# Kernel optimization log

Measured on AMD Instinct MI355X. Metric: run time of the kernel, lower is better.

## Reference

```python
import jax, jax.numpy as jnp
import numpy as np

B, S, D_MODEL, H = 4, 2048, 2048, 16
HD = D_MODEL // H  # 128
ROPE_BASE = 10000.0


def apply_rope(x):
    # x: [B, H, S, HD]; interleaved-pair rotary embedding along seq axis
    s, d = x.shape[2], x.shape[3]
    inv_freq = 1.0 / (ROPE_BASE ** (jnp.arange(0, d, 2, dtype=jnp.float32) / d))  # [d/2]
    ang = jnp.arange(s, dtype=jnp.float32)[:, None] * inv_freq[None, :]  # [S, d/2]
    cos, sin = jnp.cos(ang), jnp.sin(ang)
    x0, x1 = x[..., 0::2], x[..., 1::2]  # [B,H,S,d/2]
    o0 = x0 * cos - x1 * sin
    o1 = x0 * sin + x1 * cos
    return jnp.stack([o0, o1], axis=-1).reshape(x.shape)


def setup_inputs() -> dict:
    key = jax.random.key(0)
    ks = jax.random.split(key, 5)
    sc = 1.0 / np.sqrt(D_MODEL)
    return {
        "x": jax.random.normal(ks[0], (B, S, D_MODEL), dtype=jnp.float32),
        "Wq": jax.random.normal(ks[1], (D_MODEL, D_MODEL), dtype=jnp.float32) * sc,
        "Wk": jax.random.normal(ks[2], (D_MODEL, D_MODEL), dtype=jnp.float32) * sc,
        "Wv": jax.random.normal(ks[3], (D_MODEL, D_MODEL), dtype=jnp.float32) * sc,
        "Wo": jax.random.normal(ks[4], (D_MODEL, D_MODEL), dtype=jnp.float32) * sc,
        "bo": jnp.zeros((D_MODEL,), dtype=jnp.float32),
    }


def reference(x, Wq, Wk, Wv, Wo, bo):
    b, s, _ = x.shape
    # torch Linear: y = x @ W.T (no qkv bias)
    q = (x @ Wq.T).reshape(b, s, H, HD).transpose(0, 2, 1, 3)  # [B,H,S,HD]
    k = (x @ Wk.T).reshape(b, s, H, HD).transpose(0, 2, 1, 3)
    v = (x @ Wv.T).reshape(b, s, H, HD).transpose(0, 2, 1, 3)
    q = apply_rope(q)
    k = apply_rope(k)
    scores = jnp.einsum("bhqd,bhkd->bhqk", q, k)
    causal = jnp.tril(jnp.ones((s, s), dtype=bool))
    scores = jnp.where(causal, scores, -jnp.inf)
    attn = jax.nn.softmax(scores / jnp.sqrt(jnp.float32(HD)), axis=-1)
    # dropout p=0.0 -> identity
    ctx = jnp.einsum("bhqk,bhkd->bqhd", attn, v).reshape(b, s, H * HD)
    return ctx @ Wo.T + bo
```

## Files before the change

### kernel.cpp

```cpp
#include <hip/hip_runtime.h>
#include <hip/hip_bf16.h>
#include <math.h>

#define B_  4
#define S_  2048
#define DM  2048
#define H_  16
#define HD_ 128

typedef __bf16 bf16;
typedef __bf16 bf16x4 __attribute__((ext_vector_type(4)));
typedef __bf16 bf16x8 __attribute__((ext_vector_type(8)));
typedef float  f32x4  __attribute__((ext_vector_type(4)));

__device__ __forceinline__ void gload_lds16(const bf16* g, bf16* l) {
  __builtin_amdgcn_global_load_lds(
      (const __attribute__((address_space(1))) void*)g,
      (__attribute__((address_space(3))) void*)l, 16, 0, 0);
}

#define NX4 4194304
#define NW4 1048576
__global__ void cast_all(const float* __restrict__ x, const float* __restrict__ wq,
                         const float* __restrict__ wk, const float* __restrict__ wv,
                         const float* __restrict__ wo,
                         bf16* __restrict__ xb, bf16* __restrict__ wqkv,
                         bf16* __restrict__ wob) {
  const int total = NX4 + 4 * NW4;
  int stride = gridDim.x * blockDim.x;
  for (int i = blockIdx.x * blockDim.x + threadIdx.x; i < total; i += stride) {
    const float* src; bf16* dst; int j;
    if (i < NX4) { src = x; dst = xb; j = i; }
    else {
      int t = i - NX4; int r = t >> 20; j = t & (NW4 - 1);
      if      (r == 0) { src = wq; dst = wqkv; }
      else if (r == 1) { src = wk; dst = wqkv + (size_t)NW4 * 4; }
      else if (r == 2) { src = wv; dst = wqkv + (size_t)NW4 * 8; }
      else             { src = wo; dst = wob; }
    }
    float4 v = reinterpret_cast<const float4*>(src)[j];
    bf16x4 o = { (bf16)v.x, (bf16)v.y, (bf16)v.z, (bf16)v.w };
    reinterpret_cast<bf16x4*>(dst)[j] = o;
  }
}

__global__ void rope_table_k(float* __restrict__ tab) {
  int idx = blockIdx.x * blockDim.x + threadIdx.x;
  if (idx >= S_ * (HD_ / 2)) return;
  int pos = idx >> 6, i = idx & 63;
  float inv = powf(10000.0f, -(2.0f * i) / (float)HD_);
  float ang = (float)pos * inv;
  tab[2 * idx]     = cosf(ang);
  tab[2 * idx + 1] = sinf(ang);
}

template<int EPI>
__global__ __launch_bounds__(512, 2)
void gemm8p(const bf16* __restrict__ A, const bf16* __restrict__ Bt,
            bf16* __restrict__ Oq, bf16* __restrict__ Ok, bf16* __restrict__ Ovt,
            float* __restrict__ Cf, const float* __restrict__ bias,
            const float* __restrict__ tab, int N, int K) {
  __shared__ char lds[131072];
  const int tid = threadIdx.x;
  const int w = tid >> 6, l = tid & 63;
  const int lr = l & 15, lg = l >> 4;
  const int wm = w >> 2, wn = w & 3;
  const int L = blockIdx.x + gridDim.x * blockIdx.y;
  const int xcd = L & 7, s = L >> 3;
  const int rpx = gridDim.y >> 3;
  const int qq_ = s / gridDim.x;
  const int by = xcd * rpx + qq_;
  const int bx = s - qq_ * gridDim.x;
  const int row0 = by * 256, col0 = bx * 256;
  const int NT = K >> 6;

  auto stageSlot = [&](int isB, int kh, int kt2) {
    const bf16* src = isB ? (Bt + (size_t)col0 * K) : (A + (size_t)row0 * K);
    char* dstbase = (char*)lds + (kt2 & 1) * 65536 + isB * 32768 + kh * 16384;
    const int kcol = kt2 * 64 + kh * 32;
#pragma unroll
    for (int u = 0; u < 2; ++u) {
      int D = w * 2048 + u * 1024 + l * 16;
      int r = D >> 6, cb = D & 63;
      int sc = cb ^ (((r >> 1) & 3) << 4);
      gload_lds16(src + (size_t)r * K + kcol + (sc >> 1),
                  (bf16*)(dstbase + w * 2048 + u * 1024));
    }
  };

  const int swzt = ((lr >> 1) & 3) << 4;
  int offA[2][4], offB[4];
#pragma unroll
  for (int qm = 0; qm < 2; ++qm)
#pragma unroll
    for (int mi = 0; mi < 4; ++mi) {
      int r = wm * 128 + qm * 64 + mi * 16 + lr;
      offA[qm][mi] = r * 64 + ((lg * 16) ^ swzt);
    }
#pragma unroll
  for (int ni = 0; ni < 4; ++ni) {
    int r = wn * 64 + ni * 16 + lr;
    offB[ni] = 32768 + r * 64 + ((lg * 16) ^ swzt);
  }

  f32x4 acc[8][4] = {};

  stageSlot(0, 0, 0); stageSlot(1, 0, 0);
  stageSlot(0, 1, 0); stageSlot(1, 1, 0);
  if (NT > 1) { stageSlot(0, 0, 1); stageSlot(1, 0, 1); }

#pragma unroll 1
  for (int kt = 0; kt < NT; ++kt) {
    const char* bufb = (const char*)lds + (kt & 1) * 65536;
#pragma unroll
    for (int q = 0; q < 4; ++q) {
      const int kh = q >> 1;
      const int qmm = (q & 1);
      if (q == 0) {
        if (kt + 1 < NT) asm volatile("s_waitcnt vmcnt(8)" ::: "memory");
        else             asm volatile("s_waitcnt vmcnt(4)" ::: "memory");
        __builtin_amdgcn_s_barrier();
      } else if (q == 2) {
        if (kt + 1 < NT) asm volatile("s_waitcnt vmcnt(8)" ::: "memory");
        else             asm volatile("s_waitcnt vmcnt(0)" ::: "memory");
        __builtin_amdgcn_s_barrier();
      }
      const char* bb = bufb + kh * 16384;
      bf16x8 af[4], bfr[4];
#pragma unroll
      for (int mi = 0; mi < 4; ++mi)
        af[mi] = *reinterpret_cast<const bf16x8*>(bb + offA[qmm][mi]);
#pragma unroll
      for (int ni = 0; ni < 4; ++ni)
        bfr[ni] = *reinterpret_cast<const bf16x8*>(bb + offB[ni]);
      if (q < 2) { if (kt + 1 < NT) stageSlot(q & 1, 1, kt + 1); }
      else       { if (kt + 2 < NT) stageSlot(q & 1, 0, kt + 2); }
      __builtin_amdgcn_s_barrier();
      __builtin_amdgcn_s_setprio(1);
#pragma unroll
      for (int mi = 0; mi < 4; ++mi)
#pragma unroll
        for (int ni = 0; ni < 4; ++ni)
          acc[qmm * 4 + mi][ni] =
              __builtin_amdgcn_mfma_f32_16x16x32_bf16(af[mi], bfr[ni], acc[qmm * 4 + mi][ni], 0, 0, 0);
      __builtin_amdgcn_s_setprio(0);
    }
  }

#pragma unroll
  for (int ai = 0; ai < 8; ++ai) {
    int rb = row0 + wm * 128 + ai * 16 + lg * 4;
#pragma unroll
    for (int ni = 0; ni < 4; ++ni) {
      int gc = col0 + wn * 64 + ni * 16 + lr;
      if (EPI == 1) {
#pragma unroll
        for (int j = 0; j < 4; ++j)
          Cf[(size_t)(rb + j) * N + gc] = acc[ai][ni][j] + bias[gc];
      } else {
        int reg = col0 >> 11;
        int cc = gc & 2047;
        if (reg == 2) {
          int bb2 = rb >> 11, ss = rb & 2047;
          int hh = cc >> 7, dd = cc & 127;
          bf16x4 pack = { (bf16)acc[ai][ni][0], (bf16)acc[ai][ni][1],
                          (bf16)acc[ai][ni][2], (bf16)acc[ai][ni][3] };
          *reinterpret_cast<bf16x4*>(Ovt + (((size_t)(bb2 * H_ + hh) * HD_ + dd) << 11) + ss) = pack;
        } else {
          bf16* Dst = (reg == 0) ? Oq : Ok;
          float scale = (reg == 0) ? 0.08838834764831845f : 1.0f;
          int i2 = (cc & 127) >> 1;
          float sgn = (lr & 1) ? 1.0f : -1.0f;
#pragma unroll
          for (int j = 0; j < 4; ++j) {
            float own = acc[ai][ni][j];
            float par = __shfl_xor(own, 1);
            int ss = (rb + j) & (S_ - 1);
            float2 cs = reinterpret_cast<const float2*>(tab)[ss * 64 + i2];
            Dst[(size_t)(rb + j) * 2048 + cc] = (bf16)((own * cs.x + sgn * par * cs.y) * scale);
          }
        }
      }
    }
  }
}

__global__ __launch_bounds__(512, 4)
void attn_fwd(const bf16* __restrict__ Q, const bf16* __restrict__ K,
              const bf16* __restrict__ Vt, bf16* __restrict__ O) {
  __shared__ bf16 Ks[2][64 * 128];
  __shared__ bf16 Vs[2][128 * 64];
  __shared__ bf16 Ps[8][16 * 64];
  const int tid = threadIdx.x;
  const int w = tid >> 6, l = tid & 63;
  const int lr = l & 15, lg = l >> 4;
  const int L = blockIdx.x + 8 * (blockIdx.y + 16 * blockIdx.z);
  const int xcd = L & 7, s = L >> 3;
  const int p = xcd * 8 + (s & 7);
  const int bx = s >> 3;
  const int h = p & 15, b = p >> 4;
  const size_t bbase = (size_t)b * S_ * DM + (size_t)h * HD_;
  const bf16* vtb = Vt + (size_t)(b * H_ + h) * HD_ * S_;

#pragma unroll 1
  for (int pass = 0; pass < 2; ++pass) {
    const int qt = pass ? bx : (15 - bx);
    const int q0 = qt * 128 + w * 16;
    const int ktmax = 2 * qt + 1;

    bf16x8 qf[4];
#pragma unroll
    for (int kb = 0; kb < 4; ++kb)
      qf[kb] = *reinterpret_cast<const bf16x8*>(Q + bbase + (size_t)(q0 + lr) * DM + kb * 32 + lg * 8);

    float m_r = -INFINITY;
    float l_r = 0.f;
    f32x4 o[8] = {};

#pragma unroll
    for (int i = 0; i < 2; ++i) {
      int X = w * 2048 + i * 1024 + l * 16;
      int r = X >> 8, scb = (X & 255) ^ ((r & 7) << 4);
      gload_lds16(K + bbase + (size_t)r * DM + (scb >> 1), &Ks[0][(w * 2048 + i * 1024) >> 1]);
    }
#pragma unroll
    for (int i = 0; i < 2; ++i) {
      int X = w * 2048 + i * 1024 + l * 16;
      int d = X >> 7, scb = (X & 127) ^ ((d & 7) << 4);
      gload_lds16(vtb + (size_t)d * S_ + (scb >> 1), &Vs[0][(w * 2048 + i * 1024) >> 1]);
    }

    for (int kt = 0; kt <= ktmax; ++kt) {
      const int buf = kt & 1;
      if (kt < ktmax) {
        const int nk = (kt + 1) * 64;
#pragma unroll
        for (int i = 0; i < 2; ++i) {
          int X = w * 2048 + i * 1024 + l * 16;
          int r = X >> 8, scb = (X & 255) ^ ((r & 7) << 4);
          gload_lds16(K + bbase + (size_t)(nk + r) * DM + (scb >> 1),
                      &Ks[buf ^ 1][(w * 2048 + i * 1024) >> 1]);
        }
#pragma unroll
        for (int i = 0; i < 2; ++i) {
          int X = w * 2048 + i * 1024 + l * 16;
          int d = X >> 7, scb = (X & 127) ^ ((d & 7) << 4);
          gload_lds16(vtb + (size_t)d * S_ + nk + (scb >> 1),
                      &Vs[buf ^ 1][(w * 2048 + i * 1024) >> 1]);
        }
        asm volatile("s_waitcnt vmcnt(4)" ::: "memory");
      } else {
        asm volatile("s_waitcnt vmcnt(0)" ::: "memory");
      }
      __builtin_amdgcn_s_barrier();

      f32x4 sc4[4];
      __builtin_amdgcn_s_setprio(1);
#pragma unroll
      for (int cb = 0; cb < 4; ++cb) {
        sc4[cb] = f32x4{0.f, 0.f, 0.f, 0.f};
        int r = cb * 16 + lr;
#pragma unroll
        for (int kb = 0; kb < 4; ++kb) {
          int off = r * 256 + ((kb * 64 + lg * 16) ^ ((lr & 7) << 4));
          bf16x8 kf = *reinterpret_cast<const bf16x8*>((const char*)Ks[buf] + off);
          sc4[cb] = __builtin_amdgcn_mfma_f32_16x16x32_bf16(kf, qf[kb], sc4[cb], 0, 0, 0);
        }
      }
      __builtin_amdgcn_s_setprio(0);

      const int kv0 = kt * 64;
      if (kv0 + 63 > q0) {
        const int qq = q0 + lr;
#pragma unroll
        for (int cb = 0; cb < 4; ++cb)
#pragma unroll
          for (int jj = 0; jj < 4; ++jj)
            if (kv0 + cb * 16 + lg * 4 + jj > qq) sc4[cb][jj] = -INFINITY;
      }

      float tm = -INFINITY;
#pragma unroll
      for (int cb = 0; cb < 4; ++cb)
#pragma unroll
        for (int jj = 0; jj < 4; ++jj) tm = fmaxf(tm, sc4[cb][jj]);
      tm = fmaxf(tm, __shfl_xor(tm, 16));
      tm = fmaxf(tm, __shfl_xor(tm, 32));
      const bool resc = !__all(tm <= m_r + 8.0f);
      float sc_f = 1.f;
      if (resc) {
        float mnew = fmaxf(m_r, tm);
        sc_f = __expf(m_r - mnew);
        m_r = mnew;
      }
      float rs = 0.f;
#pragma unroll
      for (int cb = 0; cb < 4; ++cb)
#pragma unroll
        for (int jj = 0; jj < 4; ++jj) {
          float pp = __expf(sc4[cb][jj] - m_r);
          sc4[cb][jj] = pp;
          rs += pp;
        }
      rs += __shfl_xor(rs, 16);
      rs += __shfl_xor(rs, 32);
      l_r = l_r * sc_f + rs;
      if (resc) {
        float scO[4];
#pragma unroll
        for (int j = 0; j < 4; ++j) scO[j] = __shfl(sc_f, lg * 4 + j);
#pragma unroll
        for (int nb = 0; nb < 8; ++nb)
#pragma unroll
          for (int j = 0; j < 4; ++j) o[nb][j] *= scO[j];
      }

#pragma unroll
      for (int cb = 0; cb < 4; ++cb) {
        bf16x4 pk = { (bf16)sc4[cb][0], (bf16)sc4[cb][1], (bf16)sc4[cb][2], (bf16)sc4[cb][3] };
        int off = lr * 128 + ((cb * 32 + lg * 8) ^ ((lr & 7) << 4));
        *reinterpret_cast<bf16x4*>((char*)Ps[w] + off) = pk;
      }

      bf16x8 pf[2];
#pragma unroll
      for (int kc = 0; kc < 2; ++kc) {
        int off = lr * 128 + ((kc * 64 + lg * 16) ^ ((lr & 7) << 4));
        pf[kc] = *reinterpret_cast<const bf16x8*>((const char*)Ps[w] + off);
      }
      __builtin_amdgcn_s_setprio(1);
#pragma unroll
      for (int nb = 0; nb < 8; ++nb) {
        int d = nb * 16 + lr;
#pragma unroll
        for (int kc = 0; kc < 2; ++kc) {
          int off = d * 128 + ((kc * 64 + lg * 16) ^ ((lr & 7) << 4));
          bf16x8 vf = *reinterpret_cast<const bf16x8*>((const char*)Vs[buf] + off);
          o[nb] = __builtin_amdgcn_mfma_f32_16x16x32_bf16(pf[kc], vf, o[nb], 0, 0, 0);
        }
      }
      __builtin_amdgcn_s_setprio(0);

      asm volatile("s_waitcnt lgkmcnt(0)" ::: "memory");
      __builtin_amdgcn_s_barrier();
    }

    float lO[4];
#pragma unroll
    for (int j = 0; j < 4; ++j) lO[j] = __shfl(l_r, lg * 4 + j);
#pragma unroll
    for (int j = 0; j < 4; ++j) {
      float inv = 1.0f / lO[j];
      size_t rowoff = bbase + (size_t)(q0 + lg * 4 + j) * DM;
#pragma unroll
      for (int nb = 0; nb < 8; ++nb)
        O[rowoff + nb * 16 + lr] = (bf16)(o[nb][j] * inv);
    }
  }
}

extern "C" void kernel_launch(void* const* d_in, const int* in_sizes, int n_in,
                              void* d_out, int out_size, void* d_ws, size_t ws_size,
                              hipStream_t stream) {
  const float* x  = (const float*)d_in[0];
  const float* Wq = (const float*)d_in[1];
  const float* Wk = (const float*)d_in[2];
  const float* Wv = (const float*)d_in[3];
  const float* Wo = (const float*)d_in[4];
  const float* bo = (const float*)d_in[5];
  float* out = (float*)d_out;

  const size_t NX = (size_t)B_ * S_ * DM;
  const size_t NW = (size_t)DM * DM;
  char* ws = (char*)d_ws;
  bf16* xb   = (bf16*)ws; ws += NX * 2;
  bf16* wqkv = (bf16*)ws; ws += 3 * NW * 2;
  bf16* wob  = (bf16*)ws; ws += NW * 2;
  bf16* qb   = (bf16*)ws; ws += NX * 2;
  bf16* kb   = (bf16*)ws; ws += NX * 2;
  bf16* vt   = (bf16*)ws; ws += NX * 2;
  bf16* ctxb = (bf16*)ws; ws += NX * 2;
  float* tab = (float*)ws; ws += (size_t)S_ * 64 * 2 * sizeof(float);

  cast_all<<<2048, 256, 0, stream>>>(x, Wq, Wk, Wv, Wo, xb, wqkv, wob);
  rope_table_k<<<(S_ * 64 + 255) / 256, 256, 0, stream>>>(tab);

  const int M = B_ * S_;
  gemm8p<0><<<dim3(3 * DM / 256, M / 256), 512, 0, stream>>>(
      xb, wqkv, qb, kb, vt, nullptr, nullptr, tab, 3 * DM, DM);

  attn_fwd<<<dim3(8, H_, B_), 512, 0, stream>>>(qb, kb, vt, ctxb);

  gemm8p<1><<<dim3(DM / 256, M / 256), 512, 0, stream>>>(
      ctxb, wob, nullptr, nullptr, nullptr, out, bo, nullptr, DM, DM);
}
```

Baseline: 418.4 us.

## Switch GEMMs to 32x32x16 MFMA with full-K-tile staging and simpler pipeline

Both projection GEMMs now use 32x32x16 bf16 MFMA tiles instead of 16x16x32, which cuts the number of LDS fragment reads per MFMA. Each K-tile of 64 is staged as a whole, with a 128-byte row swizzle and a simpler two-phase double buffer. The XCD-aware block remapping is dropped in favour of plain blockIdx ordering. The trade-off is less prefetch depth (one tile ahead instead of two half-tiles) and possibly worse L2 locality, since blocks are no longer grouped per XCD.

```diff
diff --git a/kernel.cpp b/kernel.cpp
--- a/kernel.cpp
+++ b/kernel.cpp
@@ -12,6 +12,7 @@
 typedef __bf16 bf16x4 __attribute__((ext_vector_type(4)));
 typedef __bf16 bf16x8 __attribute__((ext_vector_type(8)));
 typedef float  f32x4  __attribute__((ext_vector_type(4)));
+typedef float  f32x16 __attribute__((ext_vector_type(16)));
 
 __device__ __forceinline__ void gload_lds16(const bf16* g, bf16* l) {
   __builtin_amdgcn_global_load_lds(
@@ -56,133 +57,133 @@
 
 template<int EPI>
 __global__ __launch_bounds__(512, 2)
-void gemm8p(const bf16* __restrict__ A, const bf16* __restrict__ Bt,
+void gemm32(const bf16* __restrict__ A, const bf16* __restrict__ Bt,
             bf16* __restrict__ Oq, bf16* __restrict__ Ok, bf16* __restrict__ Ovt,
             float* __restrict__ Cf, const float* __restrict__ bias,
             const float* __restrict__ tab, int N, int K) {
   __shared__ char lds[131072];
   const int tid = threadIdx.x;
   const int w = tid >> 6, l = tid & 63;
-  const int lr = l & 15, lg = l >> 4;
+  const int l31 = l & 31, lh = l >> 5;
   const int wm = w >> 2, wn = w & 3;
-  const int L = blockIdx.x + gridDim.x * blockIdx.y;
-  const int xcd = L & 7, s = L >> 3;
-  const int rpx = gridDim.y >> 3;
-  const int qq_ = s / gridDim.x;
-  const int by = xcd * rpx + qq_;
-  const int bx = s - qq_ * gridDim.x;
-  const int row0 = by * 256, col0 = bx * 256;
+  const int row0 = blockIdx.y * 256, col0 = blockIdx.x * 256;
   const int NT = K >> 6;
 
-  auto stageSlot = [&](int isB, int kh, int kt2) {
+  auto stageOp = [&](int isB, int kt2) {
     const bf16* src = isB ? (Bt + (size_t)col0 * K) : (A + (size_t)row0 * K);
-    char* dstbase = (char*)lds + (kt2 & 1) * 65536 + isB * 32768 + kh * 16384;
-    const int kcol = kt2 * 64 + kh * 32;
-#pragma unroll
-    for (int u = 0; u < 2; ++u) {
-      int D = w * 2048 + u * 1024 + l * 16;
-      int r = D >> 6, cb = D & 63;
-      int sc = cb ^ (((r >> 1) & 3) << 4);
-      gload_lds16(src + (size_t)r * K + kcol + (sc >> 1),
-                  (bf16*)(dstbase + w * 2048 + u * 1024));
+    char* dst = (char*)lds + (kt2 & 1) * 65536 + isB * 32768 + w * 4096;
+    const int kc = kt2 * 64;
+#pragma unroll
+    for (int g = 0; g < 4; ++g) {
+      int D = w * 4096 + g * 1024 + l * 16;
+      int r = D >> 7, cb = D & 127;
+      int sc = cb ^ ((r & 7) << 4);
+      gload_lds16(src + (size_t)r * K + kc + (sc >> 1), (bf16*)(dst + g * 1024));
     }
   };
 
-  const int swzt = ((lr >> 1) & 3) << 4;
-  int offA[2][4], offB[4];
-#pragma unroll
-  for (int qm = 0; qm < 2; ++qm)
-#pragma unroll
-    for (int mi = 0; mi < 4; ++mi) {
-      int r = wm * 128 + qm * 64 + mi * 16 + lr;
-      offA[qm][mi] = r * 64 + ((lg * 16) ^ swzt);
-    }
-#pragma unroll
-  for (int ni = 0; ni < 4; ++ni) {
-    int r = wn * 64 + ni * 16 + lr;
-    offB[ni] = 32768 + r * 64 + ((lg * 16) ^ swzt);
-  }
-
-  f32x4 acc[8][4] = {};
-
-  stageSlot(0, 0, 0); stageSlot(1, 0, 0);
-  stageSlot(0, 1, 0); stageSlot(1, 1, 0);
-  if (NT > 1) { stageSlot(0, 0, 1); stageSlot(1, 0, 1); }
+  int rA[4], sA[4], rB[2], sB[2];
+#pragma unroll
+  for (int mi = 0; mi < 4; ++mi) {
+    int r = wm * 128 + mi * 32 + l31;
+    rA[mi] = r * 128; sA[mi] = (r & 7) << 4;
+  }
+#pragma unroll
+  for (int ni = 0; ni < 2; ++ni) {
+    int r = wn * 64 + ni * 32 + l31;
+    rB[ni] = 32768 + r * 128; sB[ni] = (r & 7) << 4;
+  }
+  const int kbase = lh * 16;
+
+  f32x16 acc[4][2] = {};
+
+  stageOp(0, 0); stageOp(1, 0);
 
 #pragma unroll 1
   for (int kt = 0; kt < NT; ++kt) {
     const char* bufb = (const char*)lds + (kt & 1) * 65536;
 #pragma unroll
-    for (int q = 0; q < 4; ++q) {
-      const int kh = q >> 1;
-      const int qmm = (q & 1);
-      if (q == 0) {
-        if (kt + 1 < NT) asm volatile("s_waitcnt vmcnt(8)" ::: "memory");
-        else             asm volatile("s_waitcnt vmcnt(4)" ::: "memory");
+    for (int p = 0; p < 2; ++p) {
+      if (p == 0) {
+        if (kt + 1 < NT) { stageOp(0, kt + 1); asm volatile("s_waitcnt vmcnt(4)" ::: "memory"); }
+        else             { asm volatile("s_waitcnt vmcnt(0)" ::: "memory"); }
         __builtin_amdgcn_s_barrier();
-      } else if (q == 2) {
-        if (kt + 1 < NT) asm volatile("s_waitcnt vmcnt(8)" ::: "memory");
-        else             asm volatile("s_waitcnt vmcnt(0)" ::: "memory");
-        __builtin_amdgcn_s_barrier();
-      }
-      const char* bb = bufb + kh * 16384;
-      bf16x8 af[4], bfr[4];
+      } else {
+        if (kt + 1 < NT) stageOp(1, kt + 1);
+      }
+      bf16x8 af[4][2], bfv[2][2];
 #pragma unroll
       for (int mi = 0; mi < 4; ++mi)
-        af[mi] = *reinterpret_cast<const bf16x8*>(bb + offA[qmm][mi]);
-#pragma unroll
-      for (int ni = 0; ni < 4; ++ni)
-        bfr[ni] = *reinterpret_cast<const bf16x8*>(bb + offB[ni]);
-      if (q < 2) { if (kt + 1 < NT) stageSlot(q & 1, 1, kt + 1); }
-      else       { if (kt + 2 < NT) stageSlot(q & 1, 0, kt + 2); }
-      __builtin_amdgcn_s_barrier();
+#pragma unroll
+        for (int ks = 0; ks < 2; ++ks)
+          af[mi][ks] = *reinterpret_cast<const bf16x8*>(
+              bufb + rA[mi] + ((p * 64 + ks * 32 + kbase) ^ sA[mi]));
+#pragma unroll
+      for (int ni = 0; ni < 2; ++ni)
+#pragma unroll
+        for (int ks = 0; ks < 2; ++ks)
+          bfv[ni][ks] = *reinterpret_cast<const bf16x8*>(
+              bufb + rB[ni] + ((p * 64 + ks * 32 + kbase) ^ sB[ni]));
       __builtin_amdgcn_s_setprio(1);
 #pragma unroll
       for (int mi = 0; mi < 4; ++mi)
 #pragma unroll
-        for (int ni = 0; ni < 4; ++ni)
-          acc[qmm * 4 + mi][ni] =
-              __builtin_amdgcn_mfma_f32_16x16x32_bf16(af[mi], bfr[ni], acc[qmm * 4 + mi][ni], 0, 0, 0);
+        for (int ni = 0; ni < 2; ++ni)
+#pragma unroll
+          for (int ks = 0; ks < 2; ++ks)
+            acc[mi][ni] = __builtin_amdgcn_mfma_f32_32x32x16_bf16(
+                af[mi][ks], bfv[ni][ks], acc[mi][ni], 0, 0, 0);
       __builtin_amdgcn_s_setprio(0);
-    }
-  }
-
-#pragma unroll
-  for (int ai = 0; ai < 8; ++ai) {
-    int rb = row0 + wm * 128 + ai * 16 + lg * 4;
-#pragma unroll
-    for (int ni = 0; ni < 4; ++ni) {
-      int gc = col0 + wn * 64 + ni * 16 + lr;
+      if (p == 1) __builtin_amdgcn_s_barrier();
+    }
+  }
+
+#pragma unroll
+  for (int mi = 0; mi < 4; ++mi)
+#pragma unroll
+    for (int ni = 0; ni < 2; ++ni) {
+      int gc = col0 + wn * 64 + ni * 32 + l31;
       if (EPI == 1) {
 #pragma unroll
-        for (int j = 0; j < 4; ++j)
-          Cf[(size_t)(rb + j) * N + gc] = acc[ai][ni][j] + bias[gc];
+        for (int g = 0; g < 4; ++g) {
+          int rbase = row0 + wm * 128 + mi * 32 + 8 * g + 4 * lh;
+#pragma unroll
+          for (int j = 0; j < 4; ++j)
+            Cf[(size_t)(rbase + j) * N + gc] = acc[mi][ni][4 * g + j] + bias[gc];
+        }
       } else {
         int reg = col0 >> 11;
         int cc = gc & 2047;
         if (reg == 2) {
-          int bb2 = rb >> 11, ss = rb & 2047;
           int hh = cc >> 7, dd = cc & 127;
-          bf16x4 pack = { (bf16)acc[ai][ni][0], (bf16)acc[ai][ni][1],
-                          (bf16)acc[ai][ni][2], (bf16)acc[ai][ni][3] };
-          *reinterpret_cast<bf16x4*>(Ovt + (((size_t)(bb2 * H_ + hh) * HD_ + dd) << 11) + ss) = pack;
+#pragma unroll
+          for (int g = 0; g < 4; ++g) {
+            int rbase = row0 + wm * 128 + mi * 32 + 8 * g + 4 * lh;
+            int bb2 = rbase >> 11, ss = rbase & 2047;
+            bf16x4 pack = { (bf16)acc[mi][ni][4 * g], (bf16)acc[mi][ni][4 * g + 1],
+                            (bf16)acc[mi][ni][4 * g + 2], (bf16)acc[mi][ni][4 * g + 3] };
+            *reinterpret_cast<bf16x4*>(Ovt + (((size_t)(bb2 * H_ + hh) * HD_ + dd) << 11) + ss) = pack;
+          }
         } else {
           bf16* Dst = (reg == 0) ? Oq : Ok;
           float scale = (reg == 0) ? 0.08838834764831845f : 1.0f;
           int i2 = (cc & 127) >> 1;
-          float sgn = (lr & 1) ? 1.0f : -1.0f;
-#pragma unroll
-          for (int j = 0; j < 4; ++j) {
-            float own = acc[ai][ni][j];
-            float par = __shfl_xor(own, 1);
-            int ss = (rb + j) & (S_ - 1);
-            float2 cs = reinterpret_cast<const float2*>(tab)[ss * 64 + i2];
-            Dst[(size_t)(rb + j) * 2048 + cc] = (bf16)((own * cs.x + sgn * par * cs.y) * scale);
+          float sgn = (l & 1) ? 1.0f : -1.0f;
+#pragma unroll
+          for (int g = 0; g < 4; ++g) {
+            int rbase = row0 + wm * 128 + mi * 32 + 8 * g + 4 * lh;
+#pragma unroll
+            for (int j = 0; j < 4; ++j) {
+              float own = acc[mi][ni][4 * g + j];
+              float par = __shfl_xor(own, 1);
+              int ss = (rbase + j) & (S_ - 1);
+              float2 cs = reinterpret_cast<const float2*>(tab)[ss * 64 + i2];
+              Dst[(size_t)(rbase + j) * 2048 + cc] = (bf16)((own * cs.x + sgn * par * cs.y) * scale);
+            }
           }
         }
       }
     }
-  }
 }
 
 __global__ __launch_bounds__(512, 4)
@@ -386,11 +387,11 @@
   rope_table_k<<<(S_ * 64 + 255) / 256, 256, 0, stream>>>(tab);
 
   const int M = B_ * S_;
-  gemm8p<0><<<dim3(3 * DM / 256, M / 256), 512, 0, stream>>>(
+  gemm32<0><<<dim3(3 * DM / 256, M / 256), 512, 0, stream>>>(
       xb, wqkv, qb, kb, vt, nullptr, nullptr, tab, 3 * DM, DM);
 
   attn_fwd<<<dim3(8, H_, B_), 512, 0, stream>>>(qb, kb, vt, ctxb);
 
-  gemm8p<1><<<dim3(DM / 256, M / 256), 512, 0, stream>>>(
+  gemm32<1><<<dim3(DM / 256, M / 256), 512, 0, stream>>>(
       ctxb, wob, nullptr, nullptr, nullptr, out, bo, nullptr, DM, DM);
 }
```

New measurement: 422.2 us. About the same (+0.9%).

## Restructure GEMM k-loop to reuse B fragments and drop XCD block remap

Applied to the files above, without the earlier changes.

The GEMM main loop now walks two k-halves per tile instead of four quarters. Each half loads the B fragments from LDS once and reuses them for both M sub-tiles, with the A-fragment reload and the next global-to-LDS stage interleaved between the two MFMA groups. The vmcnt waits and barriers move to match the new stage order. The XCD-aware block-index remapping is replaced by plain blockIdx tiling, which may reduce L2 locality across chiplets.

```diff
diff --git a/kernel.cpp b/kernel.cpp
--- a/kernel.cpp
+++ b/kernel.cpp
@@ -56,22 +56,16 @@
 
 template<int EPI>
 __global__ __launch_bounds__(512, 2)
-void gemm8p(const bf16* __restrict__ A, const bf16* __restrict__ Bt,
-            bf16* __restrict__ Oq, bf16* __restrict__ Ok, bf16* __restrict__ Ovt,
-            float* __restrict__ Cf, const float* __restrict__ bias,
-            const float* __restrict__ tab, int N, int K) {
+void gemm16d(const bf16* __restrict__ A, const bf16* __restrict__ Bt,
+             bf16* __restrict__ Oq, bf16* __restrict__ Ok, bf16* __restrict__ Ovt,
+             float* __restrict__ Cf, const float* __restrict__ bias,
+             const float* __restrict__ tab, int N, int K) {
   __shared__ char lds[131072];
   const int tid = threadIdx.x;
   const int w = tid >> 6, l = tid & 63;
   const int lr = l & 15, lg = l >> 4;
   const int wm = w >> 2, wn = w & 3;
-  const int L = blockIdx.x + gridDim.x * blockIdx.y;
-  const int xcd = L & 7, s = L >> 3;
-  const int rpx = gridDim.y >> 3;
-  const int qq_ = s / gridDim.x;
-  const int by = xcd * rpx + qq_;
-  const int bx = s - qq_ * gridDim.x;
-  const int row0 = by * 256, col0 = bx * 256;
+  const int row0 = blockIdx.y * 256, col0 = blockIdx.x * 256;
   const int NT = K >> 6;
 
   auto stageSlot = [&](int isB, int kh, int kt2) {
@@ -108,41 +102,53 @@
   stageSlot(0, 0, 0); stageSlot(1, 0, 0);
   stageSlot(0, 1, 0); stageSlot(1, 1, 0);
   if (NT > 1) { stageSlot(0, 0, 1); stageSlot(1, 0, 1); }
+  asm volatile("s_waitcnt vmcnt(8)" ::: "memory");
+  __builtin_amdgcn_s_barrier();
 
 #pragma unroll 1
   for (int kt = 0; kt < NT; ++kt) {
     const char* bufb = (const char*)lds + (kt & 1) * 65536;
 #pragma unroll
-    for (int q = 0; q < 4; ++q) {
-      const int kh = q >> 1;
-      const int qmm = (q & 1);
-      if (q == 0) {
-        if (kt + 1 < NT) asm volatile("s_waitcnt vmcnt(8)" ::: "memory");
-        else             asm volatile("s_waitcnt vmcnt(4)" ::: "memory");
-        __builtin_amdgcn_s_barrier();
-      } else if (q == 2) {
-        if (kt + 1 < NT) asm volatile("s_waitcnt vmcnt(8)" ::: "memory");
-        else             asm volatile("s_waitcnt vmcnt(0)" ::: "memory");
-        __builtin_amdgcn_s_barrier();
-      }
+    for (int kh = 0; kh < 2; ++kh) {
       const char* bb = bufb + kh * 16384;
       bf16x8 af[4], bfr[4];
 #pragma unroll
-      for (int mi = 0; mi < 4; ++mi)
-        af[mi] = *reinterpret_cast<const bf16x8*>(bb + offA[qmm][mi]);
-#pragma unroll
       for (int ni = 0; ni < 4; ++ni)
         bfr[ni] = *reinterpret_cast<const bf16x8*>(bb + offB[ni]);
-      if (q < 2) { if (kt + 1 < NT) stageSlot(q & 1, 1, kt + 1); }
-      else       { if (kt + 2 < NT) stageSlot(q & 1, 0, kt + 2); }
+#pragma unroll
+      for (int mi = 0; mi < 4; ++mi)
+        af[mi] = *reinterpret_cast<const bf16x8*>(bb + offA[0][mi]);
+      if (kh == 0) { if (kt + 1 < NT) stageSlot(0, 1, kt + 1); }
+      else         { if (kt + 2 < NT) stageSlot(0, 0, kt + 2); }
       __builtin_amdgcn_s_barrier();
       __builtin_amdgcn_s_setprio(1);
 #pragma unroll
       for (int mi = 0; mi < 4; ++mi)
 #pragma unroll
         for (int ni = 0; ni < 4; ++ni)
-          acc[qmm * 4 + mi][ni] =
-              __builtin_amdgcn_mfma_f32_16x16x32_bf16(af[mi], bfr[ni], acc[qmm * 4 + mi][ni], 0, 0, 0);
+          acc[mi][ni] = __builtin_amdgcn_mfma_f32_16x16x32_bf16(af[mi], bfr[ni], acc[mi][ni], 0, 0, 0);
+      __builtin_amdgcn_s_setprio(0);
+#pragma unroll
+      for (int mi = 0; mi < 4; ++mi)
+        af[mi] = *reinterpret_cast<const bf16x8*>(bb + offA[1][mi]);
+      if (kh == 0) {
+        if (kt + 1 < NT) stageSlot(1, 1, kt + 1);
+        if (kt == NT - 1) asm volatile("s_waitcnt vmcnt(0)" ::: "memory");
+        else              asm volatile("s_waitcnt vmcnt(8)" ::: "memory");
+      } else {
+        if (kt + 2 < NT) stageSlot(1, 0, kt + 2);
+        if (kt < NT - 1) {
+          if (kt == NT - 2) asm volatile("s_waitcnt vmcnt(4)" ::: "memory");
+          else              asm volatile("s_waitcnt vmcnt(8)" ::: "memory");
+        }
+      }
+      __builtin_amdgcn_s_barrier();
+      __builtin_amdgcn_s_setprio(1);
+#pragma unroll
+      for (int mi = 0; mi < 4; ++mi)
+#pragma unroll
+        for (int ni = 0; ni < 4; ++ni)
+          acc[4 + mi][ni] = __builtin_amdgcn_mfma_f32_16x16x32_bf16(af[mi], bfr[ni], acc[4 + mi][ni], 0, 0, 0);
       __builtin_amdgcn_s_setprio(0);
     }
   }
@@ -386,11 +392,11 @@
   rope_table_k<<<(S_ * 64 + 255) / 256, 256, 0, stream>>>(tab);
 
   const int M = B_ * S_;
-  gemm8p<0><<<dim3(3 * DM / 256, M / 256), 512, 0, stream>>>(
+  gemm16d<0><<<dim3(3 * DM / 256, M / 256), 512, 0, stream>>>(
       xb, wqkv, qb, kb, vt, nullptr, nullptr, tab, 3 * DM, DM);
 
   attn_fwd<<<dim3(8, H_, B_), 512, 0, stream>>>(qb, kb, vt, ctxb);
 
-  gemm8p<1><<<dim3(DM / 256, M / 256), 512, 0, stream>>>(
+  gemm16d<1><<<dim3(DM / 256, M / 256), 512, 0, stream>>>(
       ctxb, wob, nullptr, nullptr, nullptr, out, bo, nullptr, DM, DM);
 }
```

Measured after the change: 402.7 us (median of 3 runs). -3.8%, faster.

## Restructure GEMM main loop into two-tile phases with register-held B fragments

Applied to the files above, without the earlier changes.

Rewrites the GEMM pipeline so each loop iteration processes two K-tiles in eight phases. B fragments stay in registers across four phases, and the LDS layout is changed to 128-byte rows with an XOR swizzle. The load schedule is staggered across phases, and the XCD-aware block remapping is removed in favour of plain blockIdx mapping. This aims to cut redundant LDS reads of B and smooth how global loads overlap with MFMA work. In exchange it adds an extra barrier and an lgkmcnt wait per phase, and may lose L2 locality from the dropped block swizzle.

```diff
diff --git a/kernel.cpp b/kernel.cpp
--- a/kernel.cpp
+++ b/kernel.cpp
@@ -56,7 +56,7 @@
 
 template<int EPI>
 __global__ __launch_bounds__(512, 2)
-void gemm8p(const bf16* __restrict__ A, const bf16* __restrict__ Bt,
+void gemm8q(const bf16* __restrict__ A, const bf16* __restrict__ Bt,
             bf16* __restrict__ Oq, bf16* __restrict__ Ok, bf16* __restrict__ Ovt,
             float* __restrict__ Cf, const float* __restrict__ bias,
             const float* __restrict__ tab, int N, int K) {
@@ -65,85 +65,92 @@
   const int w = tid >> 6, l = tid & 63;
   const int lr = l & 15, lg = l >> 4;
   const int wm = w >> 2, wn = w & 3;
-  const int L = blockIdx.x + gridDim.x * blockIdx.y;
-  const int xcd = L & 7, s = L >> 3;
-  const int rpx = gridDim.y >> 3;
-  const int qq_ = s / gridDim.x;
-  const int by = xcd * rpx + qq_;
-  const int bx = s - qq_ * gridDim.x;
-  const int row0 = by * 256, col0 = bx * 256;
+  const int row0 = blockIdx.y * 256, col0 = blockIdx.x * 256;
   const int NT = K >> 6;
 
-  auto stageSlot = [&](int isB, int kh, int kt2) {
+  auto stageHalf = [&](int isB, int hf, int t) {
     const bf16* src = isB ? (Bt + (size_t)col0 * K) : (A + (size_t)row0 * K);
-    char* dstbase = (char*)lds + (kt2 & 1) * 65536 + isB * 32768 + kh * 16384;
-    const int kcol = kt2 * 64 + kh * 32;
+    char* dst = (char*)lds + (t & 1) * 65536 + isB * 32768 + hf * 16384 + w * 2048;
+    const int kc = t * 64;
 #pragma unroll
     for (int u = 0; u < 2; ++u) {
       int D = w * 2048 + u * 1024 + l * 16;
-      int r = D >> 6, cb = D & 63;
-      int sc = cb ^ (((r >> 1) & 3) << 4);
-      gload_lds16(src + (size_t)r * K + kcol + (sc >> 1),
-                  (bf16*)(dstbase + w * 2048 + u * 1024));
+      int r = D >> 7, cb = D & 127;
+      int sc = cb ^ ((r & 7) << 4);
+      gload_lds16(src + (size_t)(hf * 128 + r) * K + kc + (sc >> 1),
+                  (bf16*)(dst + u * 1024));
     }
   };
 
-  const int swzt = ((lr >> 1) & 3) << 4;
-  int offA[2][4], offB[4];
-#pragma unroll
-  for (int qm = 0; qm < 2; ++qm)
-#pragma unroll
-    for (int mi = 0; mi < 4; ++mi) {
-      int r = wm * 128 + qm * 64 + mi * 16 + lr;
-      offA[qm][mi] = r * 64 + ((lg * 16) ^ swzt);
-    }
+  const int swz = (lr & 7) << 4;
+  int offB[4][2];
 #pragma unroll
   for (int ni = 0; ni < 4; ++ni) {
-    int r = wn * 64 + ni * 16 + lr;
-    offB[ni] = 32768 + r * 64 + ((lg * 16) ^ swzt);
+    int rh = (wn & 1) * 64 + ni * 16 + lr;
+#pragma unroll
+    for (int kk = 0; kk < 2; ++kk)
+      offB[ni][kk] = 32768 + (wn >> 1) * 16384 + rh * 128 + ((kk * 64 + lg * 16) ^ swz);
   }
 
   f32x4 acc[8][4] = {};
 
-  stageSlot(0, 0, 0); stageSlot(1, 0, 0);
-  stageSlot(0, 1, 0); stageSlot(1, 1, 0);
-  if (NT > 1) { stageSlot(0, 0, 1); stageSlot(1, 0, 1); }
+  stageHalf(0, 0, 0); stageHalf(0, 1, 0);
+  stageHalf(1, 0, 0); stageHalf(1, 1, 0);
+  stageHalf(1, 0, 1); stageHalf(1, 1, 1);
+  asm volatile("s_waitcnt vmcnt(4)" ::: "memory");
+  __builtin_amdgcn_s_barrier();
 
 #pragma unroll 1
-  for (int kt = 0; kt < NT; ++kt) {
-    const char* bufb = (const char*)lds + (kt & 1) * 65536;
-#pragma unroll
-    for (int q = 0; q < 4; ++q) {
-      const int kh = q >> 1;
-      const int qmm = (q & 1);
+  for (int t0 = 0; t0 < NT; t0 += 2) {
+    const int t1 = t0 + 1;
+    bf16x8 breg[4][2];
+#pragma unroll
+    for (int p = 0; p < 8; ++p) {
+      const int q = p & 3;
+      const char* bufb = (const char*)lds + (p >> 2) * 65536;
       if (q == 0) {
-        if (kt + 1 < NT) asm volatile("s_waitcnt vmcnt(8)" ::: "memory");
-        else             asm volatile("s_waitcnt vmcnt(4)" ::: "memory");
-        __builtin_amdgcn_s_barrier();
-      } else if (q == 2) {
-        if (kt + 1 < NT) asm volatile("s_waitcnt vmcnt(8)" ::: "memory");
+#pragma unroll
+        for (int ni = 0; ni < 4; ++ni)
+#pragma unroll
+          for (int kk = 0; kk < 2; ++kk)
+            breg[ni][kk] = *reinterpret_cast<const bf16x8*>(bufb + offB[ni][kk]);
+      }
+      bf16x8 af[2][2];
+#pragma unroll
+      for (int mi = 0; mi < 2; ++mi) {
+        int ro = wm * 16384 + (q * 32 + mi * 16 + lr) * 128;
+#pragma unroll
+        for (int kk = 0; kk < 2; ++kk)
+          af[mi][kk] = *reinterpret_cast<const bf16x8*>(bufb + ro + ((kk * 64 + lg * 16) ^ swz));
+      }
+      if      (p == 0) stageHalf(0, 0, t1);
+      else if (p == 1) stageHalf(0, 1, t1);
+      else if (p == 2) { if (t0 + 2 < NT) stageHalf(1, 0, t0 + 2); }
+      else if (p == 3) { if (t0 + 2 < NT) stageHalf(1, 1, t0 + 2); }
+      else if (p == 4) { if (t0 + 2 < NT) stageHalf(0, 0, t0 + 2); }
+      else if (p == 5) { if (t0 + 2 < NT) stageHalf(0, 1, t0 + 2); }
+      else if (p == 6) { if (t1 + 2 < NT) stageHalf(1, 0, t1 + 2); }
+      else             { if (t1 + 2 < NT) stageHalf(1, 1, t1 + 2); }
+      if (p == 3) {
+        if (t0 + 2 < NT) asm volatile("s_waitcnt vmcnt(4)" ::: "memory");
         else             asm volatile("s_waitcnt vmcnt(0)" ::: "memory");
-        __builtin_amdgcn_s_barrier();
-      }
-      const char* bb = bufb + kh * 16384;
-      bf16x8 af[4], bfr[4];
-#pragma unroll
-      for (int mi = 0; mi < 4; ++mi)
-        af[mi] = *reinterpret_cast<const bf16x8*>(bb + offA[qmm][mi]);
-#pragma unroll
-      for (int ni = 0; ni < 4; ++ni)
-        bfr[ni] = *reinterpret_cast<const bf16x8*>(bb + offB[ni]);
-      if (q < 2) { if (kt + 1 < NT) stageSlot(q & 1, 1, kt + 1); }
-      else       { if (kt + 2 < NT) stageSlot(q & 1, 0, kt + 2); }
+      } else if (p == 7 && t0 + 2 < NT) {
+        if (t1 + 2 < NT) asm volatile("s_waitcnt vmcnt(4)" ::: "memory");
+        else             asm volatile("s_waitcnt vmcnt(0)" ::: "memory");
+      }
       __builtin_amdgcn_s_barrier();
+      asm volatile("s_waitcnt lgkmcnt(0)" ::: "memory");
       __builtin_amdgcn_s_setprio(1);
 #pragma unroll
-      for (int mi = 0; mi < 4; ++mi)
+      for (int mi = 0; mi < 2; ++mi)
 #pragma unroll
         for (int ni = 0; ni < 4; ++ni)
-          acc[qmm * 4 + mi][ni] =
-              __builtin_amdgcn_mfma_f32_16x16x32_bf16(af[mi], bfr[ni], acc[qmm * 4 + mi][ni], 0, 0, 0);
+#pragma unroll
+          for (int kk = 0; kk < 2; ++kk)
+            acc[q * 2 + mi][ni] = __builtin_amdgcn_mfma_f32_16x16x32_bf16(
+                af[mi][kk], breg[ni][kk], acc[q * 2 + mi][ni], 0, 0, 0);
       __builtin_amdgcn_s_setprio(0);
+      __builtin_amdgcn_s_barrier();
     }
   }
 
@@ -386,11 +393,11 @@
   rope_table_k<<<(S_ * 64 + 255) / 256, 256, 0, stream>>>(tab);
 
   const int M = B_ * S_;
-  gemm8p<0><<<dim3(3 * DM / 256, M / 256), 512, 0, stream>>>(
+  gemm8q<0><<<dim3(3 * DM / 256, M / 256), 512, 0, stream>>>(
       xb, wqkv, qb, kb, vt, nullptr, nullptr, tab, 3 * DM, DM);
 
   attn_fwd<<<dim3(8, H_, B_), 512, 0, stream>>>(qb, kb, vt, ctxb);
 
-  gemm8p<1><<<dim3(DM / 256, M / 256), 512, 0, stream>>>(
+  gemm8q<1><<<dim3(DM / 256, M / 256), 512, 0, stream>>>(
       ctxb, wob, nullptr, nullptr, nullptr, out, bo, nullptr, DM, DM);
 }
```

Result: faster. 403.7 us (-3.5%).
